# Performance work log

Measured on AMD Instinct MI355X. Metric: run time of the kernel, lower is better.

The kernel has to match this reference:

```python
import jax, jax.numpy as jnp
import numpy as np

B, S, H = 2, 1024, 2048
NH, HD = 16, 128
L = 4  # num_prev_layers == attention_window


def _rope(x):
    # x: [..., S, D]; standard rotate-half RoPE, base 10000
    d = x.shape[-1]
    s = x.shape[-2]
    inv_freq = 1.0 / (10000.0 ** (jnp.arange(0, d, 2, dtype=jnp.float32) / d))
    freqs = jnp.outer(jnp.arange(s, dtype=jnp.float32), inv_freq)  # [S, d/2]
    cos, sin = jnp.cos(freqs), jnp.sin(freqs)
    x1, x2 = jnp.split(x, 2, axis=-1)
    return jnp.concatenate([x1 * cos - x2 * sin, x2 * cos + x1 * sin], axis=-1)


def setup_inputs() -> dict:
    key = jax.random.key(0)
    ks = jax.random.split(key, 8)
    std = 0.02
    return {
        "hidden_states": jax.random.normal(ks[0], (B, S, H), jnp.float32),
        "prev_hidden_states": jax.random.normal(ks[1], (L, B, S, H), jnp.float32),
        "Wq": jax.random.normal(ks[2], (H, NH * HD), jnp.float32) * std,
        "bq": jnp.zeros((NH * HD,), jnp.float32),
        "Wk": jax.random.normal(ks[3], (H, NH * HD), jnp.float32) * std,
        "bk": jnp.zeros((NH * HD,), jnp.float32),
        "Wv": jax.random.normal(ks[4], (H, NH * HD), jnp.float32) * std,
        "bv": jnp.zeros((NH * HD,), jnp.float32),
        "Wo": jax.random.normal(ks[5], (NH * HD, H), jnp.float32) * std,
        "bo": jnp.zeros((H,), jnp.float32),
        "Wg": jax.random.normal(ks[6], (H, L), jnp.float32) * std,
    }


def reference(hidden_states, prev_hidden_states, Wq, bq, Wk, bk, Wv, bv, Wo, bo, Wg):
    b, s, _ = hidden_states.shape
    # queries from current layer: [b, nh, s, hd], RoPE applied
    q = (hidden_states @ Wq + bq).reshape(b, s, NH, HD).transpose(0, 2, 1, 3)
    q = _rope(q)
    # keys/values from each prev layer: [L, b, nh, s, hd]
    k = (prev_hidden_states @ Wk + bk).reshape(L, b, s, NH, HD).transpose(0, 1, 3, 2, 4)
    k = _rope(k)
    v = (prev_hidden_states @ Wv + bv).reshape(L, b, s, NH, HD).transpose(0, 1, 3, 2, 4)
    # per-prev-layer attention (no mask)
    scores = jnp.einsum('bhqd,lbhkd->lbhqk', q, k) / jnp.sqrt(jnp.float32(HD))
    attn = jax.nn.softmax(scores, axis=-1)
    lo = jnp.einsum('lbhqk,lbhkd->lbhqd', attn, v)
    lo = lo.transpose(0, 1, 3, 2, 4).reshape(L, b, s, NH * HD)  # merge heads
    # softmax gate over pooled queries -> combine layer outputs
    layer_w = jax.nn.softmax(jnp.mean(hidden_states, axis=1) @ Wg, axis=-1)  # [b, L]
    out = jnp.einsum('lbsh,bl->bsh', lo, layer_w)
    return out @ Wo + bo
```

## Files before the change

### kernel.cpp

```cpp
#include <hip/hip_runtime.h>
#include <hip/hip_bf16.h>
#include <math.h>


typedef __bf16 bf16;
typedef __bf16 bf16x4v __attribute__((ext_vector_type(4)));
typedef __bf16 bf16x8 __attribute__((ext_vector_type(8)));
typedef float f32x4 __attribute__((ext_vector_type(4)));

#define DEV static __device__ __forceinline__

DEV void gload_lds16(const void* g, void* s) {
  __builtin_amdgcn_global_load_lds(
      (const __attribute__((address_space(1))) void*)g,
      (__attribute__((address_space(3))) void*)s, 16, 0, 0);
}

DEV f32x4 mfma16(bf16x8 a, bf16x8 b, f32x4 c) {
  return __builtin_amdgcn_mfma_f32_16x16x32_bf16(a, b, c, 0, 0, 0);
}

__global__ __launch_bounds__(256) void cvt_kernel(const float* __restrict__ in,
                                                  bf16* __restrict__ out, int n4) {
  int i = blockIdx.x * 256 + threadIdx.x;
  if (i >= n4) return;
  const float4 v = ((const float4*)in)[i];
  bf16x4v o;
  o.x = (bf16)v.x; o.y = (bf16)v.y; o.z = (bf16)v.z; o.w = (bf16)v.w;
  ((bf16x4v*)out)[i] = o;
}

__global__ __launch_bounds__(256) void twt_kernel(const float* __restrict__ W,
                                                  bf16* __restrict__ Wt) {
  __shared__ float tile[64][65];
  const int t = threadIdx.x;
  const int n0 = blockIdx.x * 64, k0 = blockIdx.y * 64;
#pragma unroll
  for (int ph = 0; ph < 16; ++ph) {
    int idx = ph * 256 + t, r = idx >> 6, c = idx & 63;
    tile[r][c] = W[(size_t)(k0 + r) * 2048 + n0 + c];
  }
  __syncthreads();
#pragma unroll
  for (int ph = 0; ph < 16; ++ph) {
    int idx = ph * 256 + t, r = idx >> 6, c = idx & 63;
    Wt[(size_t)(n0 + r) * 2048 + k0 + c] = (bf16)tile[c][r];
  }
}

__global__ __launch_bounds__(64) void rope_table_kernel(float* __restrict__ cosT,
                                                        float* __restrict__ sinT) {
  int s = blockIdx.x, j = threadIdx.x;
  float inv = powf(10000.0f, -(float)j * (1.0f / 64.0f));
  float a = (float)s * inv;
  cosT[s * 64 + j] = cosf(a);
  sinT[s * 64 + j] = sinf(a);
}

__global__ __launch_bounds__(256) void rope_kernel(const bf16* __restrict__ raw,
                                                   const float* __restrict__ cosT,
                                                   const float* __restrict__ sinT,
                                                   bf16* __restrict__ outp) {
  int rid = blockIdx.x * 16 + (threadIdx.x >> 4);
  int j = threadIdx.x & 15;
  int s = rid & 1023;
  const bf16* src = raw + (size_t)rid * 128 + 4 * j;
  bf16* dst = outp + (size_t)rid * 128 + 4 * j;
  bf16x4v x1 = *(const bf16x4v*)src;
  bf16x4v x2 = *(const bf16x4v*)(src + 64);
  f32x4 c = *(const f32x4*)(cosT + s * 64 + 4 * j);
  f32x4 sn = *(const f32x4*)(sinT + s * 64 + 4 * j);
  bf16x4v o1, o2;
#pragma unroll
  for (int k = 0; k < 4; ++k) {
    float a = (float)x1[k], b2 = (float)x2[k];
    o1[k] = (bf16)(a * c[k] - b2 * sn[k]);
    o2[k] = (bf16)(b2 * c[k] + a * sn[k]);
  }
  *(bf16x4v*)dst = o1;
  *(bf16x4v*)(dst + 64) = o2;
}

__global__ __launch_bounds__(256) void mean_part_kernel(const float* __restrict__ hs,
                                                        float* __restrict__ part) {
  int bc = blockIdx.x;
  int b = bc >> 3, c0 = (bc & 7) * 256;
  int ss = blockIdx.y;
  int col = c0 + threadIdx.x;
  float s = 0.f;
  for (int r = 0; r < 128; ++r)
    s += hs[((size_t)b * 1024 + ss * 128 + r) * 2048 + col];
  part[(size_t)ss * 4096 + b * 2048 + col] = s;
}

__global__ __launch_bounds__(256) void mean_fin_kernel(const float* __restrict__ part,
                                                       float* __restrict__ meanb) {
  int c = blockIdx.x * 256 + threadIdx.x;
  float s = 0.f;
#pragma unroll
  for (int j = 0; j < 8; ++j) s += part[(size_t)j * 4096 + c];
  meanb[c] = s * (1.0f / 1024.0f);
}

__global__ __launch_bounds__(256) void gate_kernel(const float* __restrict__ meanb,
                                                   const float* __restrict__ Wg,
                                                   float* __restrict__ lwout) {
  __shared__ float red[8][256];
  int t = threadIdx.x;
  float p[8];
#pragma unroll
  for (int j = 0; j < 8; ++j) p[j] = 0.f;
  for (int hh = t; hh < 2048; hh += 256) {
    float m0 = meanb[hh], m1 = meanb[2048 + hh];
#pragma unroll
    for (int ll = 0; ll < 4; ++ll) {
      float g = Wg[hh * 4 + ll];
      p[ll] += m0 * g;
      p[4 + ll] += m1 * g;
    }
  }
#pragma unroll
  for (int j = 0; j < 8; ++j) red[j][t] = p[j];
  __syncthreads();
  for (int s2 = 128; s2 > 0; s2 >>= 1) {
    if (t < s2) {
#pragma unroll
      for (int j = 0; j < 8; ++j) red[j][t] += red[j][t + s2];
    }
    __syncthreads();
  }
  if (t == 0) {
#pragma unroll
    for (int bb = 0; bb < 2; ++bb) {
      float v0 = red[bb * 4 + 0][0], v1 = red[bb * 4 + 1][0];
      float v2 = red[bb * 4 + 2][0], v3 = red[bb * 4 + 3][0];
      float mx = fmaxf(fmaxf(v0, v1), fmaxf(v2, v3));
      float e0 = __expf(v0 - mx), e1 = __expf(v1 - mx);
      float e2 = __expf(v2 - mx), e3 = __expf(v3 - mx);
      float inv = 1.0f / (e0 + e1 + e2 + e3);
      lwout[bb * 4 + 0] = e0 * inv;
      lwout[bb * 4 + 1] = e1 * inv;
      lwout[bb * 4 + 2] = e2 * inv;
      lwout[bb * 4 + 3] = e3 * inv;
    }
  }
}

template <int OUTMODE>
__global__ __launch_bounds__(256) void gemm_kernel(const bf16* __restrict__ A,
                                                   const bf16* __restrict__ Bt,
                                                   const float* __restrict__ bias,
                                                   void* __restrict__ Cout,
                                                   int M, int N, int K) {
  __shared__ __attribute__((aligned(16))) bf16 As[128 * 64];
  __shared__ __attribute__((aligned(16))) bf16 Bs[128 * 64];
  const int t = threadIdx.x;
  const int w = t >> 6, l = t & 63;
  const int lo = l & 15, hi = l >> 4;
  const int wr = w >> 1, wc = w & 1;

  f32x4 acc[4][4];
#pragma unroll
  for (int m = 0; m < 4; ++m)
#pragma unroll
    for (int n = 0; n < 4; ++n)
#pragma unroll
      for (int q = 0; q < 4; ++q) acc[m][n][q] = 0.f;

  int srow[4], scl[4];
#pragma unroll
  for (int p = 0; p < 4; ++p) {
    int id = p * 256 + t;
    int r = id >> 3, cph = id & 7;
    srow[p] = r;
    scl[p] = cph ^ (r & 7);
  }

  const bf16* Ab = A + (size_t)blockIdx.y * 128 * K;
  const bf16* Bb = Bt + (size_t)blockIdx.x * 128 * K;

  for (int kt = 0; kt < K; kt += 64) {
#pragma unroll
    for (int p = 0; p < 4; ++p)
      gload_lds16(Ab + (size_t)srow[p] * K + kt + scl[p] * 8,
                  &As[(p * 256 + w * 64) * 8]);
#pragma unroll
    for (int p = 0; p < 4; ++p)
      gload_lds16(Bb + (size_t)srow[p] * K + kt + scl[p] * 8,
                  &Bs[(p * 256 + w * 64) * 8]);
    __syncthreads();
#pragma unroll
    for (int ks = 0; ks < 2; ++ks) {
      bf16x8 af[4], bfr[4];
#pragma unroll
      for (int m = 0; m < 4; ++m) {
        int row = wr * 64 + m * 16 + lo;
        int ch = (ks * 4 + hi) ^ (row & 7);
        af[m] = *(const bf16x8*)&As[row * 64 + ch * 8];
      }
#pragma unroll
      for (int n = 0; n < 4; ++n) {
        int row = wc * 64 + n * 16 + lo;
        int ch = (ks * 4 + hi) ^ (row & 7);
        bfr[n] = *(const bf16x8*)&Bs[row * 64 + ch * 8];
      }
#pragma unroll
      for (int m = 0; m < 4; ++m)
#pragma unroll
        for (int n = 0; n < 4; ++n)
          acc[m][n] = mfma16(af[m], bfr[n], acc[m][n]);
    }
    __syncthreads();
  }

  if (OUTMODE == 2) {
#pragma unroll
    for (int m = 0; m < 4; ++m) {
#pragma unroll
      for (int i = 0; i < 4; ++i) {
        size_t row = (size_t)blockIdx.y * 128 + wr * 64 + m * 16 + hi * 4 + i;
        float rb = bias[row];
#pragma unroll
        for (int n = 0; n < 4; ++n) {
          int col = blockIdx.x * 128 + wc * 64 + n * 16 + lo;
          int pos64 = ((n >> 1) << 5) + ((lo >> 2) << 3) + ((n & 1) << 2) + (lo & 3);
          int colp = (col & ~63) | pos64;
          float v = acc[m][n][i] + rb;
          ((bf16*)Cout)[(size_t)(colp >> 10) * 2097152 + row * 1024 + (colp & 1023)] =
              (bf16)v;
        }
      }
    }
  } else {
#pragma unroll
    for (int n = 0; n < 4; ++n) {
      int col = blockIdx.x * 128 + wc * 64 + n * 16 + lo;
      float bb = bias[col];
#pragma unroll
      for (int m = 0; m < 4; ++m) {
#pragma unroll
        for (int i = 0; i < 4; ++i) {
          size_t row = (size_t)blockIdx.y * 128 + wr * 64 + m * 16 + hi * 4 + i;
          float v = acc[m][n][i] + bb;
          if (OUTMODE == 1)
            ((float*)Cout)[row * N + col] = v;
          else if (OUTMODE == 0)
            ((bf16*)Cout)[row * N + col] = (bf16)v;
          else {
            size_t g = (row >> 10) * 16 + (col >> 7);
            ((bf16*)Cout)[(g * 1024 + (row & 1023)) * 128 + (col & 127)] = (bf16)v;
          }
        }
      }
    }
  }
}

__global__ __launch_bounds__(256, 2) void attn_kernel(const bf16* __restrict__ Q,
                                                      const bf16* __restrict__ Kb,
                                                      const bf16* __restrict__ Vt,
                                                      const float* __restrict__ lw,
                                                      bf16* __restrict__ Obuf) {
  __shared__ __attribute__((aligned(16))) bf16 Ks[2][64 * 128];
  __shared__ __attribute__((aligned(16))) bf16 Vs[2][128 * 64];
  const int t = threadIdx.x, w = t >> 6, l = t & 63;
  const int lo = l & 15, hi = l >> 4;
  const int bh = blockIdx.x;
  const int qt = blockIdx.y;
  const int li = blockIdx.z;
  const int b = bh >> 4, h = bh & 15;
  const float C2 = 0.08838834764831845f * 1.44269504f;
  const float THR_RAW = 90.0f;

  bf16x8 qf[2][4];
#pragma unroll
  for (int qs = 0; qs < 2; ++qs) {
    const bf16* qptr =
        Q + ((size_t)bh * 1024 + qt * 128 + w * 32 + qs * 16 + lo) * 128;
#pragma unroll
    for (int db = 0; db < 4; ++db)
      qf[qs][db] = *(const bf16x8*)(qptr + db * 32 + hi * 8);
  }

  int krow[4], kcl[4], vrow[4], vcl[4];
#pragma unroll
  for (int p = 0; p < 4; ++p) {
    int id = p * 256 + t;
    krow[p] = id >> 4;
    kcl[p] = (id & 15) ^ (krow[p] & 7);
    vrow[p] = id >> 3;
    vcl[p] = (id & 7) ^ (vrow[p] & 7);
  }

  const bf16* Kl = Kb + ((size_t)li * 32 + bh) * (size_t)131072;
  const bf16* Vl = Vt + ((size_t)li * 32 + bh) * (size_t)131072;

  float m0 = -3e38f, m1 = -3e38f, si0 = 0.f, si1 = 0.f;
  f32x4 oacc[2][8];
#pragma unroll
  for (int qs = 0; qs < 2; ++qs)
#pragma unroll
    for (int dc = 0; dc < 8; ++dc)
#pragma unroll
      for (int q = 0; q < 4; ++q) oacc[qs][dc][q] = 0.f;

  auto stage = [&](int bi, int kt2) {
    const bf16* Ksrc = Kl + (size_t)kt2 * 8192;
#pragma unroll
    for (int p = 0; p < 4; ++p)
      gload_lds16(Ksrc + (size_t)krow[p] * 128 + kcl[p] * 8,
                  &Ks[bi][(p * 256 + w * 64) * 8]);
#pragma unroll
    for (int p = 0; p < 4; ++p)
      gload_lds16(Vl + (size_t)vrow[p] * 1024 + kt2 * 64 + vcl[p] * 8,
                  &Vs[bi][(p * 256 + w * 64) * 8]);
  };

  auto softmax_step = [&](f32x4 (&sa)[4], float& m_raw, float& si,
                          f32x4 (&oac)[8], bf16x8 (&pf2)[2]) {
    float v = sa[0][0];
#pragma unroll
    for (int kc = 0; kc < 4; ++kc)
#pragma unroll
      for (int i = 0; i < 4; ++i) v = fmaxf(v, sa[kc][i]);
    v = fmaxf(v, __shfl_xor(v, 16));
    v = fmaxf(v, __shfl_xor(v, 32));
    if (__any(v > m_raw + THR_RAW)) {
      float mn = fmaxf(m_raw, v);
      float corr = __builtin_amdgcn_exp2f((m_raw - mn) * C2);
      si *= corr;
      float cq[4];
#pragma unroll
      for (int i = 0; i < 4; ++i) cq[i] = __shfl(corr, hi * 4 + i);
#pragma unroll
      for (int dc = 0; dc < 8; ++dc)
#pragma unroll
        for (int i = 0; i < 4; ++i) oac[dc][i] *= cq[i];
      m_raw = mn;
    }
    float m2 = m_raw * C2;
    float rs = 0.f;
    bf16x4v pk[4];
#pragma unroll
    for (int kc = 0; kc < 4; ++kc) {
#pragma unroll
      for (int i = 0; i < 4; ++i) {
        float pf_ = __builtin_amdgcn_exp2f(fmaf(sa[kc][i], C2, -m2));
        rs += pf_;
        pk[kc][i] = (bf16)pf_;
      }
    }
    rs += __shfl_xor(rs, 16);
    rs += __shfl_xor(rs, 32);
    si += rs;
    pf2[0] = __builtin_shufflevector(pk[0], pk[1], 0, 1, 2, 3, 4, 5, 6, 7);
    pf2[1] = __builtin_shufflevector(pk[2], pk[3], 0, 1, 2, 3, 4, 5, 6, 7);
  };

  stage(0, 0);
  int cur = 0;
  for (int kt = 0; kt < 16; ++kt) {
    if (kt < 15) {
      stage(cur ^ 1, kt + 1);
      asm volatile("s_waitcnt vmcnt(8)" ::: "memory");
    } else {
      asm volatile("s_waitcnt vmcnt(0)" ::: "memory");
    }
    __builtin_amdgcn_s_barrier();
    __builtin_amdgcn_sched_barrier(0);

    f32x4 sa[2][4];
#pragma unroll
    for (int qs = 0; qs < 2; ++qs)
#pragma unroll
      for (int kc = 0; kc < 4; ++kc)
#pragma unroll
        for (int q = 0; q < 4; ++q) sa[qs][kc][q] = 0.f;
    __builtin_amdgcn_s_setprio(1);
#pragma unroll
    for (int kc = 0; kc < 4; ++kc) {
      int row = kc * 16 + lo;
#pragma unroll
      for (int db = 0; db < 4; ++db) {
        int ch = (db * 4 + hi) ^ (row & 7);
        bf16x8 kf = *(const bf16x8*)&Ks[cur][row * 128 + ch * 8];
        sa[0][kc] = mfma16(kf, qf[0][db], sa[0][kc]);
        sa[1][kc] = mfma16(kf, qf[1][db], sa[1][kc]);
      }
    }
    __builtin_amdgcn_s_setprio(0);

    bf16x8 pfr[2][2];
    softmax_step(sa[0], m0, si0, oacc[0], pfr[0]);
    softmax_step(sa[1], m1, si1, oacc[1], pfr[1]);

    __builtin_amdgcn_s_setprio(1);
#pragma unroll
    for (int kvc = 0; kvc < 2; ++kvc) {
#pragma unroll
      for (int dc = 0; dc < 8; ++dc) {
        int rowv = dc * 16 + lo;
        int ch = (kvc * 4 + hi) ^ (rowv & 7);
        bf16x8 vf = *(const bf16x8*)&Vs[cur][rowv * 64 + ch * 8];
        oacc[0][dc] = mfma16(pfr[0][kvc], vf, oacc[0][dc]);
        oacc[1][dc] = mfma16(pfr[1][kvc], vf, oacc[1][dc]);
      }
    }
    __builtin_amdgcn_s_setprio(0);
    __builtin_amdgcn_s_barrier();
    cur ^= 1;
  }

  float wl = lw[b * 4 + li];
#pragma unroll
  for (int qs = 0; qs < 2; ++qs) {
    float sv = (qs == 0) ? si0 : si1;
    float inv[4];
#pragma unroll
    for (int i = 0; i < 4; ++i) inv[i] = wl / __shfl(sv, hi * 4 + i);
#pragma unroll
    for (int dc = 0; dc < 8; ++dc) {
      int col = h * 128 + dc * 16 + lo;
#pragma unroll
      for (int i = 0; i < 4; ++i) {
        int srow = qt * 128 + w * 32 + qs * 16 + hi * 4 + i;
        Obuf[((size_t)(li * 2 + b) * 1024 + srow) * 2048 + col] =
            (bf16)(oacc[qs][dc][i] * inv[i]);
      }
    }
  }
}

__global__ __launch_bounds__(256) void comb_kernel(const bf16* __restrict__ Obuf,
                                                   bf16* __restrict__ comb) {
  size_t i = ((size_t)blockIdx.x * 256 + threadIdx.x) * 8;
  bf16x8 a0 = *(const bf16x8*)(Obuf + i);
  bf16x8 a1 = *(const bf16x8*)(Obuf + 4194304 + i);
  bf16x8 a2 = *(const bf16x8*)(Obuf + 8388608 + i);
  bf16x8 a3 = *(const bf16x8*)(Obuf + 12582912 + i);
  bf16x8 o;
#pragma unroll
  for (int j = 0; j < 8; ++j)
    o[j] = (bf16)((float)a0[j] + (float)a1[j] + (float)a2[j] + (float)a3[j]);
  *(bf16x8*)(comb + i) = o;
}

extern "C" void kernel_launch(void* const* d_in, const int* in_sizes, int n_in,
                              void* d_out, int out_size, void* d_ws, size_t ws_size,
                              hipStream_t stream) {
  (void)in_sizes; (void)n_in; (void)out_size; (void)ws_size;
  const float* hs = (const float*)d_in[0];
  const float* prev = (const float*)d_in[1];
  const float* Wq = (const float*)d_in[2];
  const float* bq = (const float*)d_in[3];
  const float* Wk = (const float*)d_in[4];
  const float* bk = (const float*)d_in[5];
  const float* Wv = (const float*)d_in[6];
  const float* bv = (const float*)d_in[7];
  const float* Wo = (const float*)d_in[8];
  const float* bo = (const float*)d_in[9];
  const float* Wg = (const float*)d_in[10];
  float* out = (float*)d_out;

  char* ws = (char*)d_ws;
  bf16* hs_bf = (bf16*)(ws + 0);
  bf16* prev_bf = (bf16*)(ws + 8388608);
  bf16* WqT = (bf16*)(ws + 41943040);
  bf16* WkT = (bf16*)(ws + 50331648);
  bf16* WvT = (bf16*)(ws + 58720256);
  bf16* Qraw2 = (bf16*)(ws + 67108864);
  bf16* WoT = (bf16*)(ws + 75497472);
  bf16* Kraw2 = (bf16*)(ws + 83886080);
  bf16* Vt = (bf16*)(ws + 117440512);
  float* cosT = (float*)(ws + 150994944);
  float* sinT = (float*)(ws + 151257088);
  float* part = (float*)(ws + 151519232);
  float* meanb = (float*)(ws + 151650304);
  float* lwbuf = (float*)(ws + 151666688);
  bf16* Qbf = hs_bf;
  bf16* Kbf = prev_bf;
  bf16* Obuf = Kraw2;
  bf16* comb = (bf16*)(ws + 0);

  cvt_kernel<<<4096, 256, 0, stream>>>(hs, hs_bf, 2048 * 2048 / 4);
  cvt_kernel<<<16384, 256, 0, stream>>>(prev, prev_bf, 8192 * 2048 / 4);

  twt_kernel<<<dim3(32, 32), 256, 0, stream>>>(Wq, WqT);
  twt_kernel<<<dim3(32, 32), 256, 0, stream>>>(Wk, WkT);
  twt_kernel<<<dim3(32, 32), 256, 0, stream>>>(Wv, WvT);
  twt_kernel<<<dim3(32, 32), 256, 0, stream>>>(Wo, WoT);

  rope_table_kernel<<<1024, 64, 0, stream>>>(cosT, sinT);
  mean_part_kernel<<<dim3(16, 8), 256, 0, stream>>>(hs, part);
  mean_fin_kernel<<<16, 256, 0, stream>>>(part, meanb);
  gate_kernel<<<1, 256, 0, stream>>>(meanb, Wg, lwbuf);

  gemm_kernel<3><<<dim3(16, 16), 256, 0, stream>>>(hs_bf, WqT, bq, Qraw2, 2048, 2048, 2048);
  gemm_kernel<3><<<dim3(16, 64), 256, 0, stream>>>(prev_bf, WkT, bk, Kraw2, 8192, 2048, 2048);
  gemm_kernel<2><<<dim3(64, 16), 256, 0, stream>>>(WvT, prev_bf, bv, Vt, 2048, 8192, 2048);

  rope_kernel<<<2048, 256, 0, stream>>>(Qraw2, cosT, sinT, Qbf);
  rope_kernel<<<8192, 256, 0, stream>>>(Kraw2, cosT, sinT, Kbf);

  attn_kernel<<<dim3(32, 8, 4), 256, 0, stream>>>(Qbf, Kbf, Vt, lwbuf, Obuf);

  comb_kernel<<<2048, 256, 0, stream>>>(Obuf, comb);

  gemm_kernel<1><<<dim3(16, 16), 256, 0, stream>>>(comb, WoT, bo, out, 2048, 2048, 2048);
}
```

Baseline: 417.3 us.

## Double-buffer GEMM LDS tiles and swizzle workgroup order for L2 locality

The GEMM kernel now uses two LDS buffers. It issues the global-to-LDS loads for the next K tile before computing on the current one, waiting only on the older loads through vmcnt, and it raises wave priority around the MFMA section. It also remaps the flat workgroup id so consecutive blocks share A/B tiles across XCDs, with the aim of better cache reuse. LDS use doubles to 64KB per block, which may reduce occupancy, and the swizzle assumes the workgroup count divides by 8.

```diff
diff --git a/kernel.cpp b/kernel.cpp
--- a/kernel.cpp
+++ b/kernel.cpp
@@ -152,12 +152,17 @@
                                                    const float* __restrict__ bias,
                                                    void* __restrict__ Cout,
                                                    int M, int N, int K) {
-  __shared__ __attribute__((aligned(16))) bf16 As[128 * 64];
-  __shared__ __attribute__((aligned(16))) bf16 Bs[128 * 64];
+  __shared__ __attribute__((aligned(16))) bf16 As[2][128 * 64];
+  __shared__ __attribute__((aligned(16))) bf16 Bs[2][128 * 64];
   const int t = threadIdx.x;
   const int w = t >> 6, l = t & 63;
   const int lo = l & 15, hi = l >> 4;
   const int wr = w >> 1, wc = w & 1;
+
+  const int nwg = gridDim.x * gridDim.y;
+  int flat = blockIdx.y * gridDim.x + blockIdx.x;
+  int swz = (flat & 7) * (nwg >> 3) + (flat >> 3);
+  const int bx = swz % gridDim.x, by = swz / gridDim.x;
 
   f32x4 acc[4][4];
 #pragma unroll
@@ -176,19 +181,32 @@
     scl[p] = cph ^ (r & 7);
   }
 
-  const bf16* Ab = A + (size_t)blockIdx.y * 128 * K;
-  const bf16* Bb = Bt + (size_t)blockIdx.x * 128 * K;
-
-  for (int kt = 0; kt < K; kt += 64) {
+  const bf16* Ab = A + (size_t)by * 128 * K;
+  const bf16* Bb = Bt + (size_t)bx * 128 * K;
+
+  auto stage = [&](int bi, int kt) {
 #pragma unroll
     for (int p = 0; p < 4; ++p)
       gload_lds16(Ab + (size_t)srow[p] * K + kt + scl[p] * 8,
-                  &As[(p * 256 + w * 64) * 8]);
+                  &As[bi][(p * 256 + w * 64) * 8]);
 #pragma unroll
     for (int p = 0; p < 4; ++p)
       gload_lds16(Bb + (size_t)srow[p] * K + kt + scl[p] * 8,
-                  &Bs[(p * 256 + w * 64) * 8]);
-    __syncthreads();
+                  &Bs[bi][(p * 256 + w * 64) * 8]);
+  };
+
+  stage(0, 0);
+  int cur = 0;
+  for (int kt = 0; kt < K; kt += 64) {
+    if (kt + 64 < K) {
+      stage(cur ^ 1, kt + 64);
+      asm volatile("s_waitcnt vmcnt(8)" ::: "memory");
+    } else {
+      asm volatile("s_waitcnt vmcnt(0)" ::: "memory");
+    }
+    __builtin_amdgcn_s_barrier();
+    __builtin_amdgcn_sched_barrier(0);
+    __builtin_amdgcn_s_setprio(1);
 #pragma unroll
     for (int ks = 0; ks < 2; ++ks) {
       bf16x8 af[4], bfr[4];
@@ -196,13 +214,13 @@
       for (int m = 0; m < 4; ++m) {
         int row = wr * 64 + m * 16 + lo;
         int ch = (ks * 4 + hi) ^ (row & 7);
-        af[m] = *(const bf16x8*)&As[row * 64 + ch * 8];
+        af[m] = *(const bf16x8*)&As[cur][row * 64 + ch * 8];
       }
 #pragma unroll
       for (int n = 0; n < 4; ++n) {
         int row = wc * 64 + n * 16 + lo;
         int ch = (ks * 4 + hi) ^ (row & 7);
-        bfr[n] = *(const bf16x8*)&Bs[row * 64 + ch * 8];
+        bfr[n] = *(const bf16x8*)&Bs[cur][row * 64 + ch * 8];
       }
 #pragma unroll
       for (int m = 0; m < 4; ++m)
@@ -210,7 +228,9 @@
         for (int n = 0; n < 4; ++n)
           acc[m][n] = mfma16(af[m], bfr[n], acc[m][n]);
     }
-    __syncthreads();
+    __builtin_amdgcn_s_setprio(0);
+    __builtin_amdgcn_s_barrier();
+    cur ^= 1;
   }
 
   if (OUTMODE == 2) {
@@ -218,11 +238,11 @@
     for (int m = 0; m < 4; ++m) {
 #pragma unroll
       for (int i = 0; i < 4; ++i) {
-        size_t row = (size_t)blockIdx.y * 128 + wr * 64 + m * 16 + hi * 4 + i;
+        size_t row = (size_t)by * 128 + wr * 64 + m * 16 + hi * 4 + i;
         float rb = bias[row];
 #pragma unroll
         for (int n = 0; n < 4; ++n) {
-          int col = blockIdx.x * 128 + wc * 64 + n * 16 + lo;
+          int col = bx * 128 + wc * 64 + n * 16 + lo;
           int pos64 = ((n >> 1) << 5) + ((lo >> 2) << 3) + ((n & 1) << 2) + (lo & 3);
           int colp = (col & ~63) | pos64;
           float v = acc[m][n][i] + rb;
@@ -234,13 +254,13 @@
   } else {
 #pragma unroll
     for (int n = 0; n < 4; ++n) {
-      int col = blockIdx.x * 128 + wc * 64 + n * 16 + lo;
+      int col = bx * 128 + wc * 64 + n * 16 + lo;
       float bb = bias[col];
 #pragma unroll
       for (int m = 0; m < 4; ++m) {
 #pragma unroll
         for (int i = 0; i < 4; ++i) {
-          size_t row = (size_t)blockIdx.y * 128 + wr * 64 + m * 16 + hi * 4 + i;
+          size_t row = (size_t)by * 128 + wr * 64 + m * 16 + hi * 4 + i;
           float v = acc[m][n][i] + bb;
           if (OUTMODE == 1)
             ((float*)Cout)[row * N + col] = v;
```

Result: faster. 399.7 us (-4.2%).
